# Performance work log

Hardware: AMD Instinct MI355X
Metric: run time of the kernel (lower is better)

The kernel has to match this reference:

```python
import jax, jax.numpy as jnp
import numpy as np

B, T, C, H, N_LAYER, LAYER_ID = 4, 4096, 1024, 16, 12, 1
N = C // H  # head size = 64
EPS_LN = 1e-5
EPS_GN = 1e-5 * 64


def setup_inputs() -> dict:
    key = jax.random.key(0)
    ks = jax.random.split(key, 10)
    s = 0.02  # GPT-style init scale for linear weights
    W = lambda k, shp: (jax.random.normal(k, shp, jnp.float32) * s)
    # deterministic RWKV init formulas (torch.no_grad() block)
    ddd = np.arange(C, dtype=np.float64) / C
    r01 = LAYER_ID / (N_LAYER - 1)
    r1a0 = 1.0 - LAYER_ID / N_LAYER
    hh = np.arange(H, dtype=np.float64)
    inp = dict(
        x=jax.random.normal(ks[0], (B, T, C), jnp.float32),
        ln1_w=jnp.ones((C,), jnp.float32), ln1_b=jnp.zeros((C,), jnp.float32),
        tm_maa_k=jnp.asarray(1.0 - ddd ** r1a0, jnp.float32),
        tm_maa_v=jnp.asarray(1.0 - (ddd ** r1a0 + 0.3 * r01), jnp.float32),
        tm_maa_r=jnp.asarray(1.0 - ddd ** (0.5 * r1a0), jnp.float32),
        tm_maa_g=jnp.asarray(1.0 - ddd ** (0.5 * r1a0), jnp.float32),
        tm_decay=jnp.asarray(-6.0 + 5.0 * (hh / (H - 1)) ** (0.7 + 1.3 * r01), jnp.float32),
        tm_faaaa=jnp.asarray(r01 * (1.0 - hh / (H - 1)), jnp.float32),
        Wr=W(ks[1], (C, C)), Wk=W(ks[2], (C, C)), Wv=W(ks[3], (C, C)),
        Wg=W(ks[4], (C, C)), Wo=W(ks[5], (C, C)),
        gn_w=jnp.ones((C,), jnp.float32), gn_b=jnp.zeros((C,), jnp.float32),
        ln2_w=jnp.ones((C,), jnp.float32), ln2_b=jnp.zeros((C,), jnp.float32),
        cm_maa_k=jnp.asarray(1.0 - ddd ** r1a0, jnp.float32),
        cm_maa_r=jnp.asarray(1.0 - ddd ** r1a0, jnp.float32),
        Wck=W(ks[6], (3 * C, C)), Wcv=W(ks[7], (C, 3 * C)), Wcr=W(ks[8], (C, C)),
    )
    return inp


def _layernorm(x, w, b):
    mu = x.mean(-1, keepdims=True)
    var = ((x - mu) ** 2).mean(-1, keepdims=True)
    return (x - mu) * jax.lax.rsqrt(var + EPS_LN) * w + b


def _time_shift(x):  # ZeroPad2d((0,0,1,-1)): shift right by one step in time
    return jnp.concatenate([jnp.zeros_like(x[:, :1]), x[:, :-1]], axis=1)


def _time_mix(x, maa_k, maa_v, maa_r, maa_g, decay, faaaa, Wr, Wk, Wv, Wg, Wo, gn_w, gn_b):
    xx = _time_shift(x) - x
    xk = x + xx * maa_k
    xv = x + xx * maa_v
    xr = x + xx * maa_r
    xg = x + xx * maa_g
    r = (xr @ Wr.T).reshape(B, T, H, N).transpose(0, 2, 1, 3)   # B H T N
    k = (xk @ Wk.T).reshape(B, T, H, N).transpose(0, 2, 3, 1)   # B H N T
    v = (xv @ Wv.T).reshape(B, T, H, N).transpose(0, 2, 1, 3)   # B H T N
    g = jax.nn.silu(xg @ Wg.T)                                   # B T C
    Q = 256 if T % 256 == 0 else (128 if T % 128 == 0 else T)
    w = jnp.exp(-jnp.exp(decay))                                 # (H,)
    u = faaaa                                                    # (H,)
    ws = (w ** Q).reshape(1, H, 1, 1)
    wk = (w[:, None] ** jnp.arange(Q - 1, -1, -1)[None, :]).reshape(1, H, 1, Q)
    wb = (w[:, None] ** jnp.arange(Q)[None, :]).reshape(1, H, Q, 1)
    # intra-chunk decay matrix: W[i,j] = w^(i-j-1) if i>j, u if i==j, 0 if i<j
    ii = jnp.arange(Q)[:, None]
    jj = jnp.arange(Q)[None, :]
    e = jnp.clip(ii - jj - 1, 0, None)
    Wm = jnp.where(ii > jj, w[:, None, None] ** e[None], 0.0)
    Wm = jnp.where((ii == jj)[None], u[:, None, None], Wm)[None]  # (1,H,Q,Q)
    nc = T // Q
    rr = r.reshape(B, H, nc, Q, N).transpose(2, 0, 1, 3, 4)      # nc B H Q N
    kk = k.reshape(B, H, N, nc, Q).transpose(3, 0, 1, 2, 4)      # nc B H N Q
    vv = v.reshape(B, H, nc, Q, N).transpose(2, 0, 1, 3, 4)      # nc B H Q N

    def step(state, inp):
        rc, kc, vc = inp
        a = rc @ kc                                              # B H Q Q
        y = (a * Wm) @ vc + (rc @ state) * wb                    # B H Q N
        state = ws * state + (kc * wk) @ vc                      # B H N N
        return state, y

    state0 = jnp.zeros((B, H, N, N), x.dtype)
    _, ys = jax.lax.scan(step, state0, (rr, kk, vv))
    y = ys.transpose(1, 3, 0 + 2, 0, 4) if False else ys.transpose(1, 2, 0, 3, 4).reshape(B, H, T, N)
    y = y.transpose(0, 2, 1, 3)                                  # B T H N
    # GroupNorm(H groups over C), eps = 1e-5*64
    mu = y.mean(-1, keepdims=True)
    var = ((y - mu) ** 2).mean(-1, keepdims=True)
    y = ((y - mu) * jax.lax.rsqrt(var + EPS_GN)).reshape(B, T, C) * gn_w + gn_b
    return (y * g) @ Wo.T


def _channel_mix(x, maa_k, maa_r, Wck, Wcv, Wcr):
    xx = _time_shift(x) - x
    xk = x + xx * maa_k
    xr = x + xx * maa_r
    h = jnp.square(jax.nn.relu(xk @ Wck.T))   # B T 3C
    return jax.nn.sigmoid(xr @ Wcr.T) * (h @ Wcv.T)


def reference(x, ln1_w, ln1_b, tm_maa_k, tm_maa_v, tm_maa_r, tm_maa_g, tm_decay, tm_faaaa,
              Wr, Wk, Wv, Wg, Wo, gn_w, gn_b, ln2_w, ln2_b, cm_maa_k, cm_maa_r, Wck, Wcv, Wcr):
    x = x + _time_mix(_layernorm(x, ln1_w, ln1_b), tm_maa_k, tm_maa_v, tm_maa_r, tm_maa_g,
                      tm_decay, tm_faaaa, Wr, Wk, Wv, Wg, Wo, gn_w, gn_b)
    x = x + _channel_mix(_layernorm(x, ln2_w, ln2_b), cm_maa_k, cm_maa_r, Wck, Wcv, Wcr)
    return x
```

## Files before the change

### kernel.cpp

```cpp
#include <hip/hip_runtime.h>
#include <stdint.h>

constexpr int kB  = 4;
constexpr int kT  = 4096;
constexpr int kC  = 1024;
constexpr int kH  = 16;
constexpr int kN  = 64;
constexpr int kQ  = 256;
constexpr int kNC = 16;
constexpr int kBT = kB * kT;

typedef unsigned short u16;
typedef short  s16x8 __attribute__((ext_vector_type(8)));
typedef float  f32x4 __attribute__((ext_vector_type(4)));
typedef unsigned int __attribute__((address_space(1))) u32_as1;
typedef unsigned int __attribute__((address_space(3))) u32_as3;

struct U16x4 { u16 a, b, c, d; } __attribute__((aligned(8)));

__device__ __forceinline__ float bf2f(u16 h) {
  union { unsigned int u; float f; } v; v.u = ((unsigned int)h) << 16; return v.f;
}
__device__ __forceinline__ u16 f2bf(float f) {
  union { float f; unsigned int u; } v; v.f = f;
  unsigned int r = (v.u + 0x7FFFu + ((v.u >> 16) & 1u)) >> 16;
  return (u16)r;
}
__device__ __forceinline__ f32x4 mfma16(s16x8 a, s16x8 b, f32x4 c) {
  return __builtin_amdgcn_mfma_f32_16x16x32_bf16(a, b, c, 0, 0, 0);
}
__device__ __forceinline__ void gld16(const void* g, void* l) {
  __builtin_amdgcn_global_load_lds((const u32_as1*)g, (u32_as3*)l, 16, 0, 0);
}

struct WPtrs { const float* src[12]; };

__global__ __launch_bounds__(256)
void wconv_kernel(WPtrs p, u16* __restrict__ dst) {
  int chunk = blockIdx.y;
  const float* s = p.src[chunk];
  u16* d = dst + (size_t)chunk * (kC * kC);
  int idx = (blockIdx.x * 256 + threadIdx.x) * 4;
  float4 v = *(const float4*)&s[idx];
  U16x4 o = { f2bf(v.x), f2bf(v.y), f2bf(v.z), f2bf(v.w) };
  *(U16x4*)&d[idx] = o;
}

template<int NOUT>
__global__ __launch_bounds__(256)
void ln_mix_kernel(const float* __restrict__ x,
                   const float* __restrict__ lw, const float* __restrict__ lb,
                   const float* __restrict__ m0p, const float* __restrict__ m1p,
                   const float* __restrict__ m2p, const float* __restrict__ m3p,
                   u16* __restrict__ o0, u16* __restrict__ o1,
                   u16* __restrict__ o2, u16* __restrict__ o3)
{
  int row = blockIdx.x;
  int t = row & (kT - 1);
  int tid = threadIdx.x;
  int c0 = tid * 4;
  float4 xc = *(const float4*)&x[(size_t)row * kC + c0];
  float4 xp; xp.x = 0.f; xp.y = 0.f; xp.z = 0.f; xp.w = 0.f;
  bool hasprev = (t != 0);
  if (hasprev) xp = *(const float4*)&x[(size_t)(row - 1) * kC + c0];

  float s0 = xc.x + xc.y + xc.z + xc.w;
  float q0 = xc.x*xc.x + xc.y*xc.y + xc.z*xc.z + xc.w*xc.w;
  float s1 = xp.x + xp.y + xp.z + xp.w;
  float q1 = xp.x*xp.x + xp.y*xp.y + xp.z*xp.z + xp.w*xp.w;
  #pragma unroll
  for (int off = 1; off < 64; off <<= 1) {
    s0 += __shfl_xor(s0, off); q0 += __shfl_xor(q0, off);
    s1 += __shfl_xor(s1, off); q1 += __shfl_xor(q1, off);
  }
  __shared__ float red[16];
  int wid = tid >> 6, lane = tid & 63;
  if (lane == 0) { red[wid*4+0]=s0; red[wid*4+1]=q0; red[wid*4+2]=s1; red[wid*4+3]=q1; }
  __syncthreads();
  s0 = red[0]+red[4]+red[8]+red[12];
  q0 = red[1]+red[5]+red[9]+red[13];
  s1 = red[2]+red[6]+red[10]+red[14];
  q1 = red[3]+red[7]+red[11]+red[15];
  float mu0 = s0 * (1.f/kC), v0 = q0*(1.f/kC) - mu0*mu0, rs0 = rsqrtf(v0 + 1e-5f);
  float mu1 = s1 * (1.f/kC), v1 = q1*(1.f/kC) - mu1*mu1, rs1 = rsqrtf(v1 + 1e-5f);

  float cx[4] = { xc.x, xc.y, xc.z, xc.w };
  float px[4] = { xp.x, xp.y, xp.z, xp.w };
  U16x4 w0, w1, w2, w3;
  u16* p0 = (u16*)&w0; u16* p1 = (u16*)&w1; u16* p2 = (u16*)&w2; u16* p3 = (u16*)&w3;
  #pragma unroll
  for (int j = 0; j < 4; ++j) {
    int c = c0 + j;
    float lwc = lw[c], lbc = lb[c];
    float lnc = (cx[j] - mu0) * rs0 * lwc + lbc;
    float lnp = hasprev ? (px[j] - mu1) * rs1 * lwc + lbc : 0.f;
    float d = lnp - lnc;
    p0[j] = f2bf(lnc + d * m0p[c]);
    if (NOUT >= 2) p1[j] = f2bf(lnc + d * m1p[c]);
    if (NOUT >= 4) { p2[j] = f2bf(lnc + d * m2p[c]); p3[j] = f2bf(lnc + d * m3p[c]); }
  }
  size_t ob = (size_t)row * kC + c0;
  *(U16x4*)&o0[ob] = w0;
  if (NOUT >= 2) *(U16x4*)&o1[ob] = w1;
  if (NOUT >= 4) { *(U16x4*)&o2[ob] = w2; *(U16x4*)&o3[ob] = w3; }
}

enum { EPI_BF16 = 0, EPI_RESID = 1, EPI_RELU2 = 2, EPI_SIGMOID = 3,
       EPI_FINAL0 = 4, EPI_FINALACC = 5 };

#define LOAD_A(mh, bfv)                                                       \
  _Pragma("unroll") for (int mf = 0; mf < 4; ++mf)                            \
    _Pragma("unroll") for (int ks = 0; ks < 2; ++ks)                          \
      Ar[mf][ks] = *(const s16x8*)&As[bfv][mh][                               \
          (wm2*64 + mf*16 + lo)*64 + 8*((ks*4 + q) ^ (lo & 7))];

#define LOAD_B(dst, nh, bfv)                                                  \
  _Pragma("unroll") for (int nf = 0; nf < 2; ++nf)                            \
    _Pragma("unroll") for (int ks = 0; ks < 2; ++ks)                          \
      dst[nf][ks] = *(const s16x8*)&Bs[bfv][nh][                              \
          (wn2*32 + nf*16 + lo)*64 + 8*((ks*4 + q) ^ (lo & 7))];

#define MFMA_Q(p, Bsrc)                                                       \
  __builtin_amdgcn_s_setprio(1);                                              \
  _Pragma("unroll") for (int mf = 0; mf < 4; ++mf)                            \
    _Pragma("unroll") for (int nf = 0; nf < 2; ++nf)                          \
      _Pragma("unroll") for (int ks = 0; ks < 2; ++ks)                        \
        acc[p][mf][nf] = mfma16(Ar[mf][ks], Bsrc[nf][ks], acc[p][mf][nf]);    \
  __builtin_amdgcn_s_setprio(0);

#define GWAIT(n) asm volatile("s_waitcnt vmcnt(" #n ")" ::: "memory")

template<int EPI, int LDB, int KDIM = 1024, int LDC = 1024>
__global__ __launch_bounds__(512, 2)
void gemm256(const u16* __restrict__ A, const u16* __restrict__ Wt,
             void* __restrict__ out, const float* __restrict__ resid,
             const u16* __restrict__ sigb)
{
  constexpr int NT = KDIM / 64;
  __shared__ u16 As[2][2][128 * 64];
  __shared__ u16 Bs[2][2][128 * 64];

  const int tid = threadIdx.x;
  const int w = tid >> 6, lane = tid & 63;
  const int lo = lane & 15, q = lane >> 4;
  const int wm2 = w >> 2, wn2 = w & 3;

  const int nwg = gridDim.x * gridDim.y;
  const int orig = blockIdx.y * gridDim.x + blockIdx.x;
  const int cpx = nwg >> 3;
  const int wg = (orig & 7) * cpx + (orig >> 3);
  const int n0 = (wg % gridDim.x) * 256;
  const int m0 = (wg / gridDim.x) * 256;

  const int srow = lane >> 3;
  const int sch  = (lane & 7) ^ srow;

  const u16* Ag = A  + (size_t)m0 * KDIM;
  const u16* Bg = Wt + (size_t)n0 * LDB;

  f32x4 acc[4][4][2] = {};

  auto stageA = [&](int bf, int kt, int h) {
    const u16* src = Ag + (size_t)(h*128 + w*8 + srow) * KDIM + kt*64 + 8*sch;
    u16* dst = &As[bf][h][(w*8) * 64];
    gld16(src, dst);
    gld16(src + (size_t)64 * KDIM, dst + 64*64);
  };
  auto stageB = [&](int bf, int kt, int h) {
    const u16* src = Bg + (size_t)(h*128 + w*8 + srow) * LDB + kt*64 + 8*sch;
    u16* dst = &Bs[bf][h][(w*8) * 64];
    gld16(src, dst);
    gld16(src + (size_t)64 * LDB, dst + 64*64);
  };

  stageA(0, 0, 0); stageB(0, 0, 0); stageB(0, 0, 1); stageA(0, 0, 1);

  s16x8 Ar[4][2];
  s16x8 Br0[2][2], Br1[2][2];

  for (int t = 0; t < NT - 1; ++t) {
    int bf = t & 1, nb = bf ^ 1;
    GWAIT(4);
    __builtin_amdgcn_s_barrier();
    stageA(nb, t + 1, 0);
    LOAD_A(0, bf) LOAD_B(Br0, 0, bf)
    MFMA_Q(0, Br0)
    GWAIT(4);
    __builtin_amdgcn_s_barrier();
    stageB(nb, t + 1, 0);
    LOAD_B(Br1, 1, bf)
    MFMA_Q(1, Br1)
    GWAIT(4);
    __builtin_amdgcn_s_barrier();
    stageB(nb, t + 1, 1);
    LOAD_A(1, bf)
    MFMA_Q(2, Br1)
    stageA(nb, t + 1, 1);
    MFMA_Q(3, Br0)
  }
  {
    constexpr int bf = (NT - 1) & 1;
    GWAIT(4);
    __builtin_amdgcn_s_barrier();
    LOAD_A(0, bf) LOAD_B(Br0, 0, bf)
    MFMA_Q(0, Br0)
    GWAIT(2);
    __builtin_amdgcn_s_barrier();
    LOAD_B(Br1, 1, bf)
    MFMA_Q(1, Br1)
    GWAIT(0);
    __builtin_amdgcn_s_barrier();
    LOAD_A(1, bf)
    MFMA_Q(2, Br1)
    MFMA_Q(3, Br0)
  }

  constexpr int MHq[4] = {0, 0, 1, 1}, NHq[4] = {0, 1, 1, 0};
  #pragma unroll
  for (int p = 0; p < 4; ++p) {
    #pragma unroll
    for (int mf = 0; mf < 4; ++mf) {
      #pragma unroll
      for (int nf = 0; nf < 2; ++nf) {
        #pragma unroll
        for (int rg = 0; rg < 4; ++rg) {
          int row = m0 + MHq[p]*128 + wm2*64 + mf*16 + q*4 + rg;
          int col = n0 + NHq[p]*128 + wn2*32 + nf*16 + lo;
          size_t idx = (size_t)row * LDC + col;
          float v = acc[p][mf][nf][rg];
          if (EPI == EPI_BF16) {
            ((u16*)out)[idx] = f2bf(v);
          } else if (EPI == EPI_RESID) {
            ((float*)out)[idx] = resid[idx] + v;
          } else if (EPI == EPI_RELU2) {
            float tv = v > 0.f ? v : 0.f;
            ((u16*)out)[idx] = f2bf(tv * tv);
          } else if (EPI == EPI_SIGMOID) {
            ((u16*)out)[idx] = f2bf(1.f / (1.f + __expf(-v)));
          } else if (EPI == EPI_FINAL0) {
            float s = bf2f(sigb[idx]);
            ((float*)out)[idx] = resid[idx] + s * v;
          } else {
            float s = bf2f(sigb[idx]);
            ((float*)out)[idx] += s * v;
          }
        }
      }
    }
  }
}

template<bool DECAY>
__global__ __launch_bounds__(256)
void transpose_nt(const u16* __restrict__ src, const float* __restrict__ decay,
                  u16* __restrict__ dst)
{
  __shared__ u16 tile[64][72];
  int t0 = blockIdx.x * 64;
  int h  = blockIdx.y;
  int b  = blockIdx.z;
  int tid = threadIdx.x;
  int lrow = tid >> 3;
  int lcol = (tid & 7) * 8;
  float ed = DECAY ? __expf(decay[h]) : 0.f;

  #pragma unroll
  for (int rr = 0; rr < 2; ++rr) {
    int tr = lrow + rr * 32;
    *(uint4*)&tile[tr][lcol] =
        *(const uint4*)&src[((size_t)(b*kT + t0 + tr)) * kC + h*64 + lcol];
  }
  __syncthreads();
  #pragma unroll
  for (int rr = 0; rr < 2; ++rr) {
    int n = lrow + rr * 32;
    u16 o[8] __attribute__((aligned(16)));
    #pragma unroll
    for (int j = 0; j < 8; ++j) {
      int tglob = t0 + lcol + j;
      float v = bf2f(tile[lcol + j][n]);
      if (DECAY) v *= __expf(-ed * (float)(kQ - 1 - (tglob & (kQ - 1))));
      o[j] = f2bf(v);
    }
    *(uint4*)&dst[((size_t)((b*kH + h)*64 + n)) * kT + t0 + lcol] = *(uint4*)o;
  }
}

__global__ __launch_bounds__(256)
void schunk_kernel(const u16* __restrict__ kTw, const u16* __restrict__ vT,
                   u16* __restrict__ SinitT)
{
  __shared__ u16 kls[64 * 136];
  __shared__ u16 vls[64 * 136];
  int blk = blockIdx.x;
  int c = blk & (kNC - 1), bh = blk >> 4;
  int tid = threadIdx.x, w = tid >> 6, lane = tid & 63;
  int lo = lane & 15, q = lane >> 4;
  const u16* kg = kTw + (size_t)bh * 64 * kT;
  const u16* vg = vT  + (size_t)bh * 64 * kT;
  f32x4 acc[4] = {};
  for (int half = 0; half < 2; ++half) {
    __syncthreads();
    #pragma unroll
    for (int it = 0; it < 4; ++it) {
      int row = it*16 + (tid >> 4);
      int c8  = (tid & 15) * 8;
      size_t gcol = (size_t)c * kQ + half*128 + c8;
      *(uint4*)&kls[row*136 + c8] = *(const uint4*)&kg[(size_t)row * kT + gcol];
      *(uint4*)&vls[row*136 + c8] = *(const uint4*)&vg[(size_t)row * kT + gcol];
    }
    __syncthreads();
    #pragma unroll
    for (int ks = 0; ks < 4; ++ks) {
      s16x8 av = *(const s16x8*)&vls[(w*16 + lo)*136 + ks*32 + q*8];
      #pragma unroll
      for (int nt = 0; nt < 4; ++nt) {
        s16x8 bv = *(const s16x8*)&kls[(nt*16 + lo)*136 + ks*32 + q*8];
        acc[nt] = mfma16(av, bv, acc[nt]);
      }
    }
  }
  u16* ob = SinitT + ((size_t)bh * kNC + c) * 4096;
  #pragma unroll
  for (int nt = 0; nt < 4; ++nt)
    #pragma unroll
    for (int rg = 0; rg < 4; ++rg)
      ob[(w*16 + q*4 + rg) * 64 + nt*16 + lo] = f2bf(acc[nt][rg]);
}

__global__ __launch_bounds__(256)
void sscan_kernel(const float* __restrict__ decay, u16* __restrict__ SinitT)
{
  int bh = blockIdx.x;
  int h = bh & (kH - 1);
  float wQ = __expf(-__expf(decay[h]) * (float)kQ);
  u16* base = SinitT + ((size_t)bh * kNC) * 4096 + threadIdx.x * 16;
  float S[16];
  #pragma unroll
  for (int i = 0; i < 16; ++i) S[i] = 0.f;
  for (int c = 0; c < kNC; ++c) {
    u16* p = base + (size_t)c * 4096;
    u16 tmp[16] __attribute__((aligned(16)));
    *(uint4*)&tmp[0] = *(const uint4*)p;
    *(uint4*)&tmp[8] = *(const uint4*)(p + 8);
    u16 outv[16] __attribute__((aligned(16)));
    #pragma unroll
    for (int i = 0; i < 16; ++i) {
      outv[i] = f2bf(S[i]);
      S[i] = wQ * S[i] + bf2f(tmp[i]);
    }
    *(uint4*)p = *(uint4*)&outv[0];
    *(uint4*)(p + 8) = *(uint4*)&outv[8];
  }
}

__global__ __launch_bounds__(256, 3)
void wkv_y_kernel(const u16* __restrict__ r, const u16* __restrict__ k,
                  const u16* __restrict__ vT, const u16* __restrict__ SinitT,
                  const u16* __restrict__ gpre, const float* __restrict__ decay,
                  const float* __restrict__ faaaa, const float* __restrict__ gnw,
                  const float* __restrict__ gnb, u16* __restrict__ yg)
{
  __shared__ u16 kls[2][64 * 64];
  __shared__ u16 vls[2][64 * 64];
  __shared__ u16 pbuf[64 * 72];
  __shared__ float wpow[kQ];

  int blk = blockIdx.x;
  int chunk = blk & (kNC - 1), bh = blk >> 4;
  int b = bh >> 4, h = bh & (kH - 1);
  int tid = threadIdx.x, w = tid >> 6, lane = tid & 63;
  int lo = lane & 15, q = lane >> 4;
  int t0 = chunk * kQ;
  float ed = __expf(decay[h]);
  wpow[tid] = __expf(-ed * (float)tid);
  float uu = faaaa[h];

  const size_t rbase = ((size_t)(b*kT + t0)) * kC + h*64;

  const int srow = lane >> 3;
  const int scol = 8 * ((lane & 7) ^ srow);
  const u16* kg0 = k  + ((size_t)(b*kT + t0)) * kC + h*64;
  const u16* vg0 = vT + ((size_t)(bh*64)) * kT + t0;

  auto stage = [&](int dstbuf, int jb_) {
    const u16* kgj = kg0 + (size_t)(jb_*64) * kC;
    const u16* vgj = vg0 + jb_*64;
    #pragma unroll
    for (int it = 0; it < 2; ++it) {
      int ci  = it*4 + w;
      int row = ci*8 + srow;
      gld16(kgj + (size_t)row * kC + scol, &kls[dstbuf][ci*512]);
      gld16(vgj + (size_t)row * kT + scol, &vls[dstbuf][ci*512]);
    }
  };

  stage(0, 0);

  s16x8 af[4][2];
  #pragma unroll
  for (int mt = 0; mt < 4; ++mt)
    #pragma unroll
    for (int ks = 0; ks < 2; ++ks)
      af[mt][ks] = *(const s16x8*)&r[rbase + (size_t)(mt*64 + w*16 + lo)*kC + ks*32 + q*8];

  f32x4 y[4][4] = {};
  {
    const u16* Sg = SinitT + (size_t)blk * 4096;
    #pragma unroll
    for (int ks = 0; ks < 2; ++ks) {
      s16x8 bf[4];
      #pragma unroll
      for (int nt = 0; nt < 4; ++nt)
        bf[nt] = *(const s16x8*)&Sg[(nt*16 + lo)*64 + ks*32 + q*8];
      #pragma unroll
      for (int mt = 0; mt < 4; ++mt)
        #pragma unroll
        for (int nt = 0; nt < 4; ++nt)
          y[mt][nt] = mfma16(af[mt][ks], bf[nt], y[mt][nt]);
    }
  }
  __syncthreads();

  #pragma unroll
  for (int mt = 0; mt < 4; ++mt)
    #pragma unroll
    for (int rg = 0; rg < 4; ++rg) {
      float wb = wpow[mt*64 + w*16 + q*4 + rg];
      #pragma unroll
      for (int nt = 0; nt < 4; ++nt) y[mt][nt][rg] *= wb;
    }

  u16* P = &pbuf[(w * 16) * 72];
  int buf = 0;
  #pragma unroll
  for (int jb = 0; jb < 4; ++jb) {
    if (jb < 3) stage(buf ^ 1, jb + 1);
    #pragma unroll
    for (int mt = jb; mt < 4; ++mt) {
      f32x4 a[4] = {};
      #pragma unroll
      for (int ks = 0; ks < 2; ++ks)
        #pragma unroll
        for (int nt = 0; nt < 4; ++nt) {
          s16x8 kf = *(const s16x8*)&kls[buf][(nt*16 + lo)*64 + 8*((ks*4 + q) ^ (lo & 7))];
          a[nt] = mfma16(af[mt][ks], kf, a[nt]);
        }
      #pragma unroll
      for (int nt = 0; nt < 4; ++nt)
        #pragma unroll
        for (int rg = 0; rg < 4; ++rg) {
          int i = mt*64 + w*16 + q*4 + rg;
          int j = jb*64 + nt*16 + lo;
          int d = i - j;
          float val = (d > 0) ? a[nt][rg] * wpow[d-1] : (d == 0 ? a[nt][rg] * uu : 0.f);
          P[(q*4 + rg)*72 + nt*16 + lo] = f2bf(val);
        }
      #pragma unroll
      for (int ks = 0; ks < 2; ++ks) {
        s16x8 pf = *(const s16x8*)&P[lo*72 + ks*32 + q*8];
        #pragma unroll
        for (int nt = 0; nt < 4; ++nt) {
          s16x8 vf = *(const s16x8*)&vls[buf][(nt*16 + lo)*64 + 8*((ks*4 + q) ^ (lo & 7))];
          y[mt][nt] = mfma16(pf, vf, y[mt][nt]);
        }
      }
    }
    __syncthreads();
    buf ^= 1;
  }

  float gw[4], gb[4];
  #pragma unroll
  for (int nt = 0; nt < 4; ++nt) {
    gw[nt] = gnw[h*64 + nt*16 + lo];
    gb[nt] = gnb[h*64 + nt*16 + lo];
  }
  for (int mt = 0; mt < 4; ++mt) {
    #pragma unroll
    for (int rg = 0; rg < 4; ++rg) {
      float s  = y[mt][0][rg] + y[mt][1][rg] + y[mt][2][rg] + y[mt][3][rg];
      float ss = y[mt][0][rg]*y[mt][0][rg] + y[mt][1][rg]*y[mt][1][rg]
               + y[mt][2][rg]*y[mt][2][rg] + y[mt][3][rg]*y[mt][3][rg];
      #pragma unroll
      for (int off = 1; off < 16; off <<= 1) {
        s  += __shfl_xor(s, off);
        ss += __shfl_xor(ss, off);
      }
      float mu  = s * (1.f/64.f);
      float var = ss * (1.f/64.f) - mu*mu;
      float rstd = rsqrtf(var + 6.4e-4f);
      #pragma unroll
      for (int nt = 0; nt < 4; ++nt) {
        float val = (y[mt][nt][rg] - mu) * rstd * gw[nt] + gb[nt];
        pbuf[(w*16 + q*4 + rg)*72 + nt*16 + lo] = f2bf(val);
      }
    }
    __syncthreads();
    #pragma unroll
    for (int it = 0; it < 2; ++it) {
      int lrow = it*32 + (tid >> 3);
      int c8  = (tid & 7) * 8;
      size_t ga = rbase + (size_t)(mt*64 + lrow)*kC + c8;
      uint2 ylo = *(const uint2*)&pbuf[lrow*72 + c8];
      uint2 yhi = *(const uint2*)&pbuf[lrow*72 + c8 + 4];
      uint4 gv = *(const uint4*)&gpre[ga];
      u16 yv[8] __attribute__((aligned(16)));
      const u16* ys = (const u16*)&ylo;
      const u16* gs = (const u16*)&gv;
      #pragma unroll
      for (int j = 0; j < 8; ++j) {
        u16 yj = (j < 4) ? ys[j] : ((const u16*)&yhi)[j-4];
        float g = bf2f(gs[j]);
        float sil = g / (1.f + __expf(-g));
        yv[j] = f2bf(bf2f(yj) * sil);
      }
      *(uint4*)&yg[ga] = *(uint4*)yv;
    }
    __syncthreads();
  }
}

extern "C" void kernel_launch(void* const* d_in, const int* in_sizes, int n_in,
                              void* d_out, int out_size, void* d_ws, size_t ws_size,
                              hipStream_t stream) {
  const size_t MB = 1024ull * 1024ull;
  if (ws_size < 192 * MB) return;

  const float* x     = (const float*)d_in[0];
  const float* ln1w  = (const float*)d_in[1];
  const float* ln1b  = (const float*)d_in[2];
  const float* tmk   = (const float*)d_in[3];
  const float* tmv   = (const float*)d_in[4];
  const float* tmr   = (const float*)d_in[5];
  const float* tmg   = (const float*)d_in[6];
  const float* decay = (const float*)d_in[7];
  const float* faaaa = (const float*)d_in[8];
  const float* Wr    = (const float*)d_in[9];
  const float* Wk    = (const float*)d_in[10];
  const float* Wv    = (const float*)d_in[11];
  const float* Wg    = (const float*)d_in[12];
  const float* Wo    = (const float*)d_in[13];
  const float* gnw   = (const float*)d_in[14];
  const float* gnb   = (const float*)d_in[15];
  const float* ln2w  = (const float*)d_in[16];
  const float* ln2b  = (const float*)d_in[17];
  const float* cmk   = (const float*)d_in[18];
  const float* cmr   = (const float*)d_in[19];
  const float* Wck   = (const float*)d_in[20];
  const float* Wcv   = (const float*)d_in[21];
  const float* Wcr   = (const float*)d_in[22];

  char* ws = (char*)d_ws;
  u16*   Wb     = (u16*)(ws +   0*MB);
  u16*   xr     = (u16*)(ws +  24*MB);
  u16*   xk     = (u16*)(ws +  56*MB);
  u16*   xv     = (u16*)(ws +  88*MB);
  u16*   xg     = (u16*)(ws + 120*MB);
  u16*   rb     = (u16*)(ws + 152*MB);
  u16*   kb     = (u16*)(ws +  24*MB);
  u16*   vb     = (u16*)(ws +  56*MB);
  u16*   gp     = (u16*)(ws +  88*MB);
  u16*   vT     = (u16*)(ws + 120*MB);
  u16*   kTw    = (u16*)(ws +  56*MB);
  u16*   SinitT = (u16*)(ws + 184*MB);
  u16*   yg     = (u16*)(ws +  56*MB);
  u16*   xck    = (u16*)(ws +  24*MB);
  u16*   xcr    = (u16*)(ws + 152*MB);
  u16*   sig    = (u16*)(ws +  56*MB);
  u16*   hbt    = (u16*)(ws +  88*MB);

  const int C2 = kC * kC;
  u16* Wr_b  = Wb + 0*(size_t)C2;
  u16* Wk_b  = Wb + 1*(size_t)C2;
  u16* Wv_b  = Wb + 2*(size_t)C2;
  u16* Wg_b  = Wb + 3*(size_t)C2;
  u16* Wo_b  = Wb + 4*(size_t)C2;
  u16* Wck_b = Wb + 5*(size_t)C2;
  u16* Wcv_b = Wb + 8*(size_t)C2;
  u16* Wcr_b = Wb + 11*(size_t)C2;

  WPtrs wp;
  wp.src[0] = Wr;  wp.src[1] = Wk;  wp.src[2] = Wv;  wp.src[3] = Wg;  wp.src[4] = Wo;
  wp.src[5] = Wck; wp.src[6] = Wck + C2; wp.src[7] = Wck + 2*(size_t)C2;
  wp.src[8] = Wcv; wp.src[9] = Wcv + C2; wp.src[10] = Wcv + 2*(size_t)C2;
  wp.src[11] = Wcr;
  wconv_kernel<<<dim3(C2/1024, 12), 256, 0, stream>>>(wp, Wb);

  ln_mix_kernel<4><<<kBT, 256, 0, stream>>>(x, ln1w, ln1b, tmr, tmk, tmv, tmg,
                                            xr, xk, xv, xg);
  gemm256<EPI_BF16, kC><<<dim3(4,64), 512, 0, stream>>>(xr, Wr_b, rb, nullptr, nullptr);
  gemm256<EPI_BF16, kC><<<dim3(4,64), 512, 0, stream>>>(xk, Wk_b, kb, nullptr, nullptr);
  gemm256<EPI_BF16, kC><<<dim3(4,64), 512, 0, stream>>>(xv, Wv_b, vb, nullptr, nullptr);
  gemm256<EPI_BF16, kC><<<dim3(4,64), 512, 0, stream>>>(xg, Wg_b, gp, nullptr, nullptr);

  transpose_nt<false><<<dim3(kT/64, kH, kB), 256, 0, stream>>>(vb, decay, vT);
  transpose_nt<true ><<<dim3(kT/64, kH, kB), 256, 0, stream>>>(kb, decay, kTw);
  schunk_kernel<<<kB*kH*kNC, 256, 0, stream>>>(kTw, vT, SinitT);
  sscan_kernel<<<kB*kH, 256, 0, stream>>>(decay, SinitT);
  wkv_y_kernel<<<kB*kH*kNC, 256, 0, stream>>>(rb, kb, vT, SinitT, gp, decay, faaaa,
                                              gnw, gnb, yg);
  gemm256<EPI_RESID, kC><<<dim3(4,64), 512, 0, stream>>>(yg, Wo_b, d_out, x, nullptr);

  ln_mix_kernel<2><<<kBT, 256, 0, stream>>>((const float*)d_out, ln2w, ln2b, cmk, cmr,
                                            nullptr, nullptr, xck, xcr, nullptr, nullptr);
  gemm256<EPI_SIGMOID, kC><<<dim3(4,64), 512, 0, stream>>>(xcr, Wcr_b, sig, nullptr, nullptr);
  for (int i = 0; i < 3; ++i)
    gemm256<EPI_RELU2, kC, 1024, 3*kC><<<dim3(4,64), 512, 0, stream>>>(
        xck, Wck_b + (size_t)i*C2, hbt + (size_t)i*kC, nullptr, nullptr);
  gemm256<EPI_FINALACC, 3*kC, 3*kC, kC><<<dim3(4,64), 512, 0, stream>>>(
      hbt, Wcv_b, (float*)d_out, nullptr, sig);
}
```

Baseline: 1.015 ms.

## Simplify GEMM prefetch pipeline and merge three FFN key GEMM launches

The GEMM main loop drops its staggered per-quarter staging. It now waits for every outstanding global-to-LDS load, issues one barrier per K-tile, and prefetches the whole next tile before running the four MFMA quarters. This removes the peeled epilogue iteration and two of the three barriers per tile, at the cost of less fine-grained overlap between loads and MFMA. Separately, the three channel-mix key GEMM launches are merged into a single launch with a 12-wide grid, which cuts launch overhead and gives more blocks per wave.

```diff
diff --git a/kernel.cpp b/kernel.cpp
--- a/kernel.cpp
+++ b/kernel.cpp
@@ -178,38 +178,18 @@
   s16x8 Ar[4][2];
   s16x8 Br0[2][2], Br1[2][2];
 
-  for (int t = 0; t < NT - 1; ++t) {
+  for (int t = 0; t < NT; ++t) {
     int bf = t & 1, nb = bf ^ 1;
-    GWAIT(4);
+    GWAIT(0);
     __builtin_amdgcn_s_barrier();
-    stageA(nb, t + 1, 0);
+    if (t + 1 < NT) {
+      stageA(nb, t + 1, 0); stageB(nb, t + 1, 0);
+      stageB(nb, t + 1, 1); stageA(nb, t + 1, 1);
+    }
     LOAD_A(0, bf) LOAD_B(Br0, 0, bf)
     MFMA_Q(0, Br0)
-    GWAIT(4);
-    __builtin_amdgcn_s_barrier();
-    stageB(nb, t + 1, 0);
     LOAD_B(Br1, 1, bf)
     MFMA_Q(1, Br1)
-    GWAIT(4);
-    __builtin_amdgcn_s_barrier();
-    stageB(nb, t + 1, 1);
-    LOAD_A(1, bf)
-    MFMA_Q(2, Br1)
-    stageA(nb, t + 1, 1);
-    MFMA_Q(3, Br0)
-  }
-  {
-    constexpr int bf = (NT - 1) & 1;
-    GWAIT(4);
-    __builtin_amdgcn_s_barrier();
-    LOAD_A(0, bf) LOAD_B(Br0, 0, bf)
-    MFMA_Q(0, Br0)
-    GWAIT(2);
-    __builtin_amdgcn_s_barrier();
-    LOAD_B(Br1, 1, bf)
-    MFMA_Q(1, Br1)
-    GWAIT(0);
-    __builtin_amdgcn_s_barrier();
     LOAD_A(1, bf)
     MFMA_Q(2, Br1)
     MFMA_Q(3, Br0)
@@ -605,9 +585,8 @@
   ln_mix_kernel<2><<<kBT, 256, 0, stream>>>((const float*)d_out, ln2w, ln2b, cmk, cmr,
                                             nullptr, nullptr, xck, xcr, nullptr, nullptr);
   gemm256<EPI_SIGMOID, kC><<<dim3(4,64), 512, 0, stream>>>(xcr, Wcr_b, sig, nullptr, nullptr);
-  for (int i = 0; i < 3; ++i)
-    gemm256<EPI_RELU2, kC, 1024, 3*kC><<<dim3(4,64), 512, 0, stream>>>(
-        xck, Wck_b + (size_t)i*C2, hbt + (size_t)i*kC, nullptr, nullptr);
+  gemm256<EPI_RELU2, kC, 1024, 3*kC><<<dim3(12,64), 512, 0, stream>>>(
+      xck, Wck_b, hbt, nullptr, nullptr);
   gemm256<EPI_FINALACC, 3*kC, 3*kC, kC><<<dim3(4,64), 512, 0, stream>>>(
       hbt, Wcv_b, (float*)d_out, nullptr, sig);
 }
```

After: 1.061 ms. +4.6%, slower.
